# Performance work log

Measured on AMD Instinct MI355X. Metric: run time of the kernel, lower is better.

## Reference

```python
import jax, jax.numpy as jnp
import numpy as np

B, S, H = 4, 16, 4096          # batch, new query tokens, hidden
NH, NKV, HD = 32, 8, 128       # query heads, kv heads, head_dim
PAST = 8192                    # cached kv length
ROPE_BASE = 10000.0


def setup_inputs() -> dict:
    key = jax.random.key(0)
    ks = jax.random.split(key, 7)
    wscale = 0.02
    hidden_states = jax.random.normal(ks[0], (B, S, H), jnp.float32)
    k_cache = jax.random.normal(ks[1], (B, PAST, NKV, HD), jnp.float32)
    v_cache = jax.random.normal(ks[2], (B, PAST, NKV, HD), jnp.float32)
    Wq = jax.random.normal(ks[3], (H, NH * HD), jnp.float32) * wscale
    Wk = jax.random.normal(ks[4], (H, NKV * HD), jnp.float32) * wscale
    Wv = jax.random.normal(ks[5], (H, NKV * HD), jnp.float32) * wscale
    Wo = jax.random.normal(ks[6], (NH * HD, H), jnp.float32) * wscale
    position_ids = PAST + jnp.tile(jnp.arange(S, dtype=jnp.int32)[None, :], (B, 1))
    return {"hidden_states": hidden_states, "k_cache": k_cache, "v_cache": v_cache,
            "Wq": Wq, "Wk": Wk, "Wv": Wv, "Wo": Wo, "position_ids": position_ids}


def _rotate_half(x):
    h = x.shape[-1] // 2
    return jnp.concatenate([-x[..., h:], x[..., :h]], axis=-1)


def reference(hidden_states, k_cache, v_cache, Wq, Wk, Wv, Wo, position_ids):
    b, s, _ = hidden_states.shape
    # projections -> [b, heads, s, hd]
    q = (hidden_states @ Wq).reshape(b, s, NH, HD).transpose(0, 2, 1, 3)
    k = (hidden_states @ Wk).reshape(b, s, NKV, HD).transpose(0, 2, 1, 3)
    v = (hidden_states @ Wv).reshape(b, s, NKV, HD).transpose(0, 2, 1, 3)
    # RoPE (LlamaRotaryEmbedding: base=10000, half-split rotate)
    inv_freq = 1.0 / (ROPE_BASE ** (jnp.arange(0, HD, 2, dtype=jnp.float32) / HD))
    ang = position_ids.astype(jnp.float32)[..., None] * inv_freq      # [b, s, hd/2]
    emb = jnp.concatenate([ang, ang], axis=-1)                        # [b, s, hd]
    cos = jnp.cos(emb)[:, None]                                       # [b, 1, s, hd]
    sin = jnp.sin(emb)[:, None]
    q = q * cos + _rotate_half(q) * sin
    k = k * cos + _rotate_half(k) * sin
    # kv-cache concat: cache stored [b, past, nkv, hd] -> [b, nkv, K, hd]
    k_all = jnp.concatenate([k_cache.transpose(0, 2, 1, 3), k], axis=2)
    v_all = jnp.concatenate([v_cache.transpose(0, 2, 1, 3), v], axis=2)
    # GQA repeat_kv (repeat_interleave along head dim)
    n_rep = NH // NKV
    k_all = jnp.repeat(k_all, n_rep, axis=1)                          # [b, NH, K, hd]
    v_all = jnp.repeat(v_all, n_rep, axis=1)
    K = k_all.shape[2]
    scale = HD ** -0.5
    scores = jnp.einsum('bhqd,bhkd->bhqk', q, k_all) * scale          # [b, NH, s, K]
    # flash varlen causal with seqlen_q < seqlen_k: bottom-right aligned mask
    allow = jnp.arange(K)[None, :] <= (K - s + jnp.arange(s))[:, None]
    scores = jnp.where(allow, scores, jnp.float32(-1e30))
    probs = jax.nn.softmax(scores, axis=-1)
    attn = jnp.einsum('bhqk,bhkd->bhqd', probs, v_all)                # [b, NH, s, hd]
    attn = attn.transpose(0, 2, 1, 3).reshape(b, s, NH * HD)
    return attn @ Wo
```

## Files before the change

kernel.cpp:

```cpp
#include <hip/hip_runtime.h>

#define BB 4
#define SS 16
#define NH 32
#define NKV 8
#define HD 128
#define PAST 8192
#define KVLEN 8208
#define KSPLIT 8
#define ASPLIT 16
#define CHUNK 513
#define NTILE 9

typedef __attribute__((ext_vector_type(8))) short short8;
typedef __attribute__((ext_vector_type(4))) float f32x4;

__device__ __forceinline__ unsigned short f2bf(float f) {
  unsigned u = __float_as_uint(f);
  u = (u + 0x7FFFu + ((u >> 16) & 1u)) >> 16;
  return (unsigned short)u;
}
__device__ __forceinline__ float bf2f(unsigned short h) {
  return __uint_as_float(((unsigned)h) << 16);
}
__device__ __forceinline__ unsigned cvtpk(float lo, float hi) {
  unsigned r;
  asm("v_cvt_pk_bf16_f32 %0, %1, %2" : "=v"(r) : "v"(lo), "v"(hi));
  return r;
}
__device__ __forceinline__ void st8(void* p, unsigned lo, unsigned hi) {
  *(unsigned long long*)p = (unsigned long long)lo | ((unsigned long long)hi << 32);
}
__device__ __forceinline__ float getc(const float4& v, int c) {
  return c == 0 ? v.x : c == 1 ? v.y : c == 2 ? v.z : v.w;
}
__device__ __forceinline__ int imin(int a, int b) { return a < b ? a : b; }
__device__ __forceinline__ int imax(int a, int b) { return a > b ? a : b; }

__device__ __forceinline__ void bar_lds() {
  asm volatile("s_waitcnt lgkmcnt(0)" ::: "memory");
  __builtin_amdgcn_s_barrier();
  asm volatile("" ::: "memory");
}
__device__ __forceinline__ void wait_lds() {
  asm volatile("s_waitcnt lgkmcnt(0)" ::: "memory");
}

__global__ __launch_bounds__(256) void xconv(const float* __restrict__ X,
                                             unsigned short* __restrict__ XB) {
  int gid = blockIdx.x * 256 + threadIdx.x;
  float4 v = *(const float4*)&X[(size_t)gid * 4];
  ushort4 pk;
  pk.x = f2bf(v.x); pk.y = f2bf(v.y); pk.z = f2bf(v.z); pk.w = f2bf(v.w);
  *(ushort4*)&XB[(size_t)gid * 4] = pk;
}

__global__ __launch_bounds__(256) void gemm_skinny(
    const unsigned short* __restrict__ A,
    const float* __restrict__ W0, const float* __restrict__ W1, const float* __restrict__ W2,
    int nw0, int nw1, int nw2,
    float* __restrict__ part, int Ntot, int kchunk) {
  __shared__ unsigned short Wt[64 * 64];
  const int nt = blockIdx.x, ks = blockIdx.y;
  const int tid = threadIdx.x, lane = tid & 63, w = tid >> 6;
  const int lr = lane & 15, lc = lane >> 4;
  const int n0 = nt * 64;
  const float* W; int wld, wcol;
  if (n0 < nw0) { W = W0; wld = nw0; wcol = n0; }
  else if (n0 < nw0 + nw1) { W = W1; wld = nw1; wcol = n0 - nw0; }
  else { W = W2; wld = nw2; wcol = n0 - nw0 - nw1; }

  f32x4 acc[4];
  #pragma unroll
  for (int mi = 0; mi < 4; ++mi)
    #pragma unroll
    for (int i = 0; i < 4; ++i) acc[mi][i] = 0.f;

  const int qn = tid & 15, qk = tid >> 4;
  const int kb0 = ks * kchunk;
  const int nkt = kchunk / 64;

  float4 wr0, wr1, wr2, wr3;
  {
    const float* wp = &W[(size_t)(kb0 + qk * 4) * wld + wcol + qn * 4];
    wr0 = *(const float4*)(wp);
    wr1 = *(const float4*)(wp + wld);
    wr2 = *(const float4*)(wp + 2 * (size_t)wld);
    wr3 = *(const float4*)(wp + 3 * (size_t)wld);
  }

  for (int kt = 0; kt < nkt; ++kt) {
    const int kb = kb0 + kt * 64;
    #pragma unroll
    for (int c = 0; c < 4; ++c) {
      const int n = qn * 4 + c;
      ushort4 pk;
      pk.x = f2bf(getc(wr0, c)); pk.y = f2bf(getc(wr1, c));
      pk.z = f2bf(getc(wr2, c)); pk.w = f2bf(getc(wr3, c));
      const int byt = n * 128 + ((qk * 8) ^ ((n & 7) << 4));
      *(ushort4*)((char*)Wt + byt) = pk;
    }
    bar_lds();
    if (kt + 1 < nkt) {
      const float* wp = &W[(size_t)(kb + 64 + qk * 4) * wld + wcol + qn * 4];
      wr0 = *(const float4*)(wp);
      wr1 = *(const float4*)(wp + wld);
      wr2 = *(const float4*)(wp + 2 * (size_t)wld);
      wr3 = *(const float4*)(wp + 3 * (size_t)wld);
    }
    #pragma unroll
    for (int kh = 0; kh < 2; ++kh) {
      const int ncol = w * 16 + lr;
      short8 bf = *(const short8*)((char*)Wt + ncol * 128 + ((kh * 64 + lc * 16) ^ ((ncol & 7) << 4)));
      const int kkg = kb + kh * 32 + lc * 8;
      #pragma unroll
      for (int mi = 0; mi < 4; ++mi) {
        short8 af = *(const short8*)&A[(size_t)(mi * 16 + lr) * 4096 + kkg];
        acc[mi] = __builtin_amdgcn_mfma_f32_16x16x32_bf16(af, bf, acc[mi], 0, 0, 0);
      }
    }
    bar_lds();
  }
  #pragma unroll
  for (int mi = 0; mi < 4; ++mi)
    #pragma unroll
    for (int i = 0; i < 4; ++i) {
      const int row = mi * 16 + lc * 4 + i;
      part[((size_t)ks * 64 + row) * Ntot + n0 + w * 16 + lr] = acc[mi][i];
    }
}

__global__ __launch_bounds__(256) void proj_reduce(
    const float* __restrict__ part, const int* __restrict__ posids,
    unsigned short* __restrict__ QR, float* __restrict__ KF,
    float* __restrict__ VF) {
  __shared__ double sInv[64];
  const int tid = threadIdx.x;
  if (tid < 64)
    sInv[tid] = exp2(-(double)tid * (13.287712379549449 / 64.0));
  __syncthreads();

  const int gid = blockIdx.x * 256 + tid;
  const int j = gid & 63;
  const int hh = (gid >> 6) % 48;
  const int row = gid / 3072;
  const int b = row >> 4, s = row & 15;
  int col0; bool rope;
  if (hh < 32)      { col0 = hh * 128 + j; rope = true; }
  else if (hh < 40) { col0 = 4096 + (hh - 32) * 128 + j; rope = true; }
  else              { col0 = 5120 + (hh - 40) * 128 + j; rope = false; }
  float v0 = 0.f, v1 = 0.f;
  #pragma unroll
  for (int ks = 0; ks < KSPLIT; ++ks) {
    v0 += part[((size_t)ks * 64 + row) * 6144 + col0];
    v1 += part[((size_t)ks * 64 + row) * 6144 + col0 + 64];
  }
  float o0 = v0, o1 = v1;
  if (rope) {
    const int pos = posids[row];
    const double inv = sInv[j];
    double th = (double)pos * inv;
    const double TWO_PI = 6.283185307179586476925286766559;
    th -= floor(th / TWO_PI) * TWO_PI;
    float sv, cv;
    sincosf((float)th, &sv, &cv);
    o0 = v0 * cv - v1 * sv;
    o1 = v1 * cv + v0 * sv;
  }
  if (hh < 32) {
    const size_t didx = (((size_t)(b * 32 + hh) * 16 + s) * 128) + j;
    QR[didx] = f2bf(o0);
    QR[didx + 64] = f2bf(o1);
  } else if (hh < 40) {
    const size_t didx = (((size_t)(b * 8 + (hh - 32)) * 16 + s) * 128) + j;
    KF[didx] = o0;
    KF[didx + 64] = o1;
  } else {
    const size_t didx = (((size_t)(b * 8 + (hh - 40)) * 16 + s) * 128) + j;
    VF[didx] = o0;
    VF[didx + 64] = o1;
  }
}

__global__ __launch_bounds__(512, 2) void attn_kernel(
    const float* __restrict__ kc, const float* __restrict__ vc,
    const unsigned short* __restrict__ QR, const float* __restrict__ KF,
    const float* __restrict__ VF,
    float* __restrict__ Opart, float* __restrict__ ML) {
  __shared__ unsigned short Klds[2][64 * 136];
  __shared__ unsigned short Vt[2][128 * 64];
  __shared__ unsigned short Plds[4][16 * 72];

  const int kvh = blockIdx.x & 7, b = blockIdx.x >> 3;
  const int split = blockIdx.y;
  const int tid = threadIdx.x;
  const int kstart = split * CHUNK;

  if (tid >= 256) {
    const int ptid = tid - 256;
    const int dl = (ptid & 31) * 4;
    const int rk = ptid >> 5;
    const float* kc_base = kc + (((size_t)b * PAST) * NKV + kvh) * HD + dl;
    const float* vc_base = vc + (((size_t)b * PAST) * NKV + kvh) * HD + dl;
    const float* kf_base = KF + (((size_t)b * NKV + kvh) * SS) * HD + dl;
    const float* vf_base = VF + (((size_t)b * NKV + kvh) * SS) * HD + dl;

    auto stage = [&](int kk0, int buf) {
      float4 kpre[8];
      float4 vpre[8];
      #pragma unroll
      for (int pass = 0; pass < 8; ++pass) {
        const int kk = kk0 + pass * 8 + rk;
        const int ts = imin(imax(kk - PAST, 0), SS - 1);
        const float* p = (kk < PAST) ? (kc_base + (size_t)kk * (NKV * HD))
                                     : (kf_base + (size_t)ts * HD);
        kpre[pass] = *(const float4*)p;
      }
      #pragma unroll
      for (int j = 0; j < 8; ++j) {
        const int kk = kk0 + rk * 8 + j;
        const int ts = imin(imax(kk - PAST, 0), SS - 1);
        const float* p = (kk < PAST) ? (vc_base + (size_t)kk * (NKV * HD))
                                     : (vf_base + (size_t)ts * HD);
        vpre[j] = *(const float4*)p;
      }
      #pragma unroll
      for (int pass = 0; pass < 8; ++pass) {
        const int kr = pass * 8 + rk;
        st8((char*)&Klds[buf][0] + kr * 272 + dl * 2,
            cvtpk(kpre[pass].x, kpre[pass].y), cvtpk(kpre[pass].z, kpre[pass].w));
      }
      #pragma unroll
      for (int pp = 0; pp < 2; ++pp) {
        const int krb = rk * 8 + pp * 4;
        #pragma unroll
        for (int c = 0; c < 4; ++c) {
          const int d = dl + c;
          const int g = ((d ^ (d >> 3)) & 7) << 4;
          st8((char*)&Vt[buf][0] + d * 128 + ((krb * 2) ^ g),
              cvtpk(getc(vpre[pp * 4 + 0], c), getc(vpre[pp * 4 + 1], c)),
              cvtpk(getc(vpre[pp * 4 + 2], c), getc(vpre[pp * 4 + 3], c)));
        }
      }
    };

    stage(kstart, 0);
    bar_lds();
    for (int t = 0; t < NTILE; ++t) {
      if (t + 1 < NTILE) stage(kstart + (t + 1) * 64, (t + 1) & 1);
      bar_lds();
    }
  } else {
    const int lane = tid & 63, w = tid >> 6;
    const int lr = lane & 15, lc = lane >> 4;

    short8 qf[4];
    {
      const unsigned short* qb = QR + (((size_t)b * NH + kvh * 4 + w) * SS + lr) * HD;
      #pragma unroll
      for (int kd = 0; kd < 4; ++kd) qf[kd] = *(const short8*)(qb + kd * 32 + lc * 8);
    }

    float m_i[4], l_i[4];
    f32x4 oacc[8];
    #pragma unroll
    for (int i = 0; i < 4; ++i) { m_i[i] = -1e30f; l_i[i] = 0.f; }
    #pragma unroll
    for (int d8 = 0; d8 < 8; ++d8)
      #pragma unroll
      for (int i = 0; i < 4; ++i) oacc[d8][i] = 0.f;

    bar_lds();

    for (int t = 0; t < NTILE; ++t) {
      const int buf = t & 1;
      const int kk0 = kstart + t * 64;
      const int nvalid = imin(64, kstart + CHUNK - kk0);

      f32x4 sacc[4];
      #pragma unroll
      for (int nb = 0; nb < 4; ++nb)
        #pragma unroll
        for (int i = 0; i < 4; ++i) sacc[nb][i] = 0.f;
      #pragma unroll
      for (int kd = 0; kd < 4; ++kd) {
        #pragma unroll
        for (int nb = 0; nb < 4; ++nb) {
          const int key = nb * 16 + lr;
          short8 bf = *(const short8*)((char*)&Klds[buf][0] + key * 272 + kd * 64 + lc * 16);
          sacc[nb] = __builtin_amdgcn_mfma_f32_16x16x32_bf16(qf[kd], bf, sacc[nb], 0, 0, 0);
        }
      }

      const float scl = 0.08838834764831845f;
      float resc[4];
      #pragma unroll
      for (int i = 0; i < 4; ++i) {
        const int s = lc * 4 + i;
        float vv[4];
        #pragma unroll
        for (int nb = 0; nb < 4; ++nb) {
          const int klocal = nb * 16 + lr;
          const int kk = kk0 + klocal;
          const bool ok = (klocal < nvalid) && (kk <= PAST + s);
          vv[nb] = ok ? sacc[nb][i] * scl : -1e30f;
        }
        float mx = fmaxf(fmaxf(vv[0], vv[1]), fmaxf(vv[2], vv[3]));
        mx = fmaxf(mx, __shfl_xor(mx, 1));
        mx = fmaxf(mx, __shfl_xor(mx, 2));
        mx = fmaxf(mx, __shfl_xor(mx, 4));
        mx = fmaxf(mx, __shfl_xor(mx, 8));
        const float mnew = fmaxf(m_i[i], mx);
        const float rs = __expf(m_i[i] - mnew);
        float p0 = __expf(vv[0] - mnew), p1 = __expf(vv[1] - mnew);
        float p2 = __expf(vv[2] - mnew), p3 = __expf(vv[3] - mnew);
        float sum = p0 + p1 + p2 + p3;
        sum += __shfl_xor(sum, 1);
        sum += __shfl_xor(sum, 2);
        sum += __shfl_xor(sum, 4);
        sum += __shfl_xor(sum, 8);
        l_i[i] = l_i[i] * rs + sum;
        m_i[i] = mnew;
        resc[i] = rs;
        unsigned short* prow = &Plds[w][s * 72];
        prow[0 * 16 + lr] = f2bf(p0);
        prow[1 * 16 + lr] = f2bf(p1);
        prow[2 * 16 + lr] = f2bf(p2);
        prow[3 * 16 + lr] = f2bf(p3);
      }
      #pragma unroll
      for (int d8 = 0; d8 < 8; ++d8)
        #pragma unroll
        for (int i = 0; i < 4; ++i) oacc[d8][i] *= resc[i];

      wait_lds();

      #pragma unroll
      for (int ks2 = 0; ks2 < 2; ++ks2) {
        short8 pf = *(const short8*)((char*)&Plds[w][0] + lr * 144 + ks2 * 64 + lc * 16);
        #pragma unroll
        for (int db = 0; db < 8; ++db) {
          const int d = db * 16 + lr;
          const int g = ((d ^ (d >> 3)) & 7) << 4;
          short8 vf = *(const short8*)((char*)&Vt[buf][0] + d * 128 + ((ks2 * 64 + lc * 16) ^ g));
          oacc[db] = __builtin_amdgcn_mfma_f32_16x16x32_bf16(pf, vf, oacc[db], 0, 0, 0);
        }
      }

      bar_lds();
    }

    const size_t pbase = (((size_t)b * NKV + kvh) * ASPLIT + split) * 64;
    #pragma unroll
    for (int db = 0; db < 8; ++db)
      #pragma unroll
      for (int i = 0; i < 4; ++i) {
        const int row = w * 16 + lc * 4 + i;
        Opart[(pbase + row) * HD + db * 16 + lr] = oacc[db][i];
      }
    if (lr == 0) {
      #pragma unroll
      for (int i = 0; i < 4; ++i) {
        const int row = w * 16 + lc * 4 + i;
        ML[(pbase + row) * 2] = m_i[i];
        ML[(pbase + row) * 2 + 1] = l_i[i];
      }
    }
  }
}

__global__ __launch_bounds__(128) void combine(const float* __restrict__ Opart,
                                               const float* __restrict__ ML,
                                               unsigned short* __restrict__ AT) {
  const int rid = blockIdx.x;
  const int d = threadIdx.x;
  const int s = rid & 15, h = (rid >> 4) & 31, b = rid >> 9;
  const int kvh = h >> 2, g = h & 3;
  const int prow = g * 16 + s;
  const size_t base = ((size_t)b * NKV + kvh) * ASPLIT;
  float ms[ASPLIT], ls[ASPLIT];
  float M = -1e30f;
  #pragma unroll
  for (int sp = 0; sp < ASPLIT; ++sp) {
    ms[sp] = ML[((base + sp) * 64 + prow) * 2];
    ls[sp] = ML[((base + sp) * 64 + prow) * 2 + 1];
    M = fmaxf(M, ms[sp]);
  }
  float denom = 0.f, acc = 0.f;
  #pragma unroll
  for (int sp = 0; sp < ASPLIT; ++sp) {
    const float e = __expf(ms[sp] - M);
    denom += ls[sp] * e;
    acc += e * Opart[((base + sp) * 64 + prow) * HD + d];
  }
  AT[((size_t)(b * 16 + s)) * 4096 + h * 128 + d] = f2bf(acc / denom);
}

__global__ __launch_bounds__(256) void wo_reduce(const float* __restrict__ part,
                                                 float* __restrict__ out) {
  const int gid = blockIdx.x * 256 + threadIdx.x;
  float4 s = {0, 0, 0, 0};
  #pragma unroll
  for (int ks = 0; ks < KSPLIT; ++ks) {
    const float4 v = *(const float4*)&part[(size_t)ks * 262144 + (size_t)gid * 4];
    s.x += v.x; s.y += v.y; s.z += v.z; s.w += v.w;
  }
  *(float4*)&out[(size_t)gid * 4] = s;
}

extern "C" void kernel_launch(void* const* d_in, const int* in_sizes, int n_in,
                              void* d_out, int out_size, void* d_ws, size_t ws_size,
                              hipStream_t stream) {
  (void)in_sizes; (void)n_in; (void)out_size; (void)ws_size;
  const float* hs = (const float*)d_in[0];
  const float* kc = (const float*)d_in[1];
  const float* vc = (const float*)d_in[2];
  const float* Wq = (const float*)d_in[3];
  const float* Wk = (const float*)d_in[4];
  const float* Wv = (const float*)d_in[5];
  const float* Wo = (const float*)d_in[6];
  const int* pos = (const int*)d_in[7];
  float* out = (float*)d_out;
  char* ws = (char*)d_ws;

  unsigned short* XB = (unsigned short*)(ws);
  unsigned short* QR = (unsigned short*)(ws + 0x080000);
  float* KF = (float*)(ws + 0x100000);
  float* VF = (float*)(ws + 0x140000);
  unsigned short* AT = (unsigned short*)(ws + 0x180000);
  float* RED = (float*)(ws + 0x200000);
  float* ML  = (float*)(ws + 0x1300000);

  hipLaunchKernelGGL(xconv, dim3(256), dim3(256), 0, stream, hs, XB);
  hipLaunchKernelGGL(gemm_skinny, dim3(96, KSPLIT), dim3(256), 0, stream,
                     XB, Wq, Wk, Wv, 4096, 1024, 1024, RED, 6144, 4096 / KSPLIT);
  hipLaunchKernelGGL(proj_reduce, dim3(768), dim3(256), 0, stream, RED, pos, QR, KF, VF);
  hipLaunchKernelGGL(attn_kernel, dim3(NKV * BB, ASPLIT), dim3(512), 0, stream,
                     kc, vc, QR, KF, VF, RED, ML);
  hipLaunchKernelGGL(combine, dim3(2048), dim3(128), 0, stream, RED, ML, AT);
  hipLaunchKernelGGL(gemm_skinny, dim3(64, KSPLIT), dim3(256), 0, stream,
                     AT, Wo, Wo, Wo, 4096, 0, 0, RED, 4096, 4096 / KSPLIT);
  hipLaunchKernelGGL(wo_reduce, dim3(256), dim3(256), 0, stream, RED, out);
}
```

Baseline: 134.6 us.

## Restructure split-KV attention: 4 KV heads per block, 16-key tiles, 64 splits

The attention kernel is reorganised so each block handles four KV heads over a shorter key chunk (129 keys, 16-key tiles). The grid goes from 32x16 to 8x64 blocks, and each compute wave now owns one KV head and all four of its query heads. Partial outputs are stored as fp16 instead of fp32, which halves the partial-output traffic, and the combine kernel reduces over 64 splits instead of 16. The PV MFMA now has half of its K dimension zero-padded, which wastes tensor throughput. The extra splits also raise combine work and the ML read volume.

```diff
diff --git a/kernel.cpp b/kernel.cpp
--- a/kernel.cpp
+++ b/kernel.cpp
@@ -1,4 +1,5 @@
 #include <hip/hip_runtime.h>
+#include <hip/hip_fp16.h>
 
 #define BB 4
 #define SS 16
@@ -8,9 +9,9 @@
 #define PAST 8192
 #define KVLEN 8208
 #define KSPLIT 8
-#define ASPLIT 16
-#define CHUNK 513
-#define NTILE 9
+#define NSPLIT 64
+#define CHUNKK 129
+#define NT2 9
 
 typedef __attribute__((ext_vector_type(8))) short short8;
 typedef __attribute__((ext_vector_type(4))) float f32x4;
@@ -19,9 +20,6 @@
   unsigned u = __float_as_uint(f);
   u = (u + 0x7FFFu + ((u >> 16) & 1u)) >> 16;
   return (unsigned short)u;
-}
-__device__ __forceinline__ float bf2f(unsigned short h) {
-  return __uint_as_float(((unsigned)h) << 16);
 }
 __device__ __forceinline__ unsigned cvtpk(float lo, float hi) {
   unsigned r;
@@ -186,212 +184,228 @@
     const float* __restrict__ kc, const float* __restrict__ vc,
     const unsigned short* __restrict__ QR, const float* __restrict__ KF,
     const float* __restrict__ VF,
-    float* __restrict__ Opart, float* __restrict__ ML) {
-  __shared__ unsigned short Klds[2][64 * 136];
-  __shared__ unsigned short Vt[2][128 * 64];
-  __shared__ unsigned short Plds[4][16 * 72];
-
-  const int kvh = blockIdx.x & 7, b = blockIdx.x >> 3;
+    unsigned short* __restrict__ OP, float* __restrict__ ML) {
+  __shared__ unsigned short Klds[2][8192];
+  __shared__ unsigned short Vt[2][9248];
+  __shared__ unsigned short Plds[4][1280];
+
+  const int kvhq = blockIdx.x & 1, b = blockIdx.x >> 1;
   const int split = blockIdx.y;
   const int tid = threadIdx.x;
-  const int kstart = split * CHUNK;
+  const int kstart = split * CHUNKK;
+  const int kend = imin(kstart + CHUNKK, KVLEN);
+  const int vmax = kend - 1;
 
   if (tid >= 256) {
     const int ptid = tid - 256;
-    const int dl = (ptid & 31) * 4;
-    const int rk = ptid >> 5;
-    const float* kc_base = kc + (((size_t)b * PAST) * NKV + kvh) * HD + dl;
-    const float* vc_base = vc + (((size_t)b * PAST) * NKV + kvh) * HD + dl;
-    const float* kf_base = KF + (((size_t)b * NKV + kvh) * SS) * HD + dl;
-    const float* vf_base = VF + (((size_t)b * NKV + kvh) * SS) * HD + dl;
+    const int pw = ptid >> 6;
+    const int pl = ptid & 63;
+    const int lv = pl & 31;
+    const int hh2 = pl >> 5;
+    const int dd = lv * 4;
+
+    auto kaddr = [&](int kk, int kvl) -> const float* {
+      const int kkc = imin(kk, vmax);
+      const int kvh = kvhq * 4 + kvl;
+      if (kkc < PAST) return kc + (((size_t)b * PAST + kkc) * NKV + kvh) * HD + dd;
+      return KF + (((size_t)(b * NKV + kvh)) * SS + (kkc - PAST)) * HD + dd;
+    };
+    auto vaddr = [&](int kk, int kvl) -> const float* {
+      const int kkc = imin(kk, vmax);
+      const int kvh = kvhq * 4 + kvl;
+      if (kkc < PAST) return vc + (((size_t)b * PAST + kkc) * NKV + kvh) * HD + dd;
+      return VF + (((size_t)(b * NKV + kvh)) * SS + (kkc - PAST)) * HD + dd;
+    };
 
     auto stage = [&](int kk0, int buf) {
-      float4 kpre[8];
-      float4 vpre[8];
-      #pragma unroll
-      for (int pass = 0; pass < 8; ++pass) {
-        const int kk = kk0 + pass * 8 + rk;
-        const int ts = imin(imax(kk - PAST, 0), SS - 1);
-        const float* p = (kk < PAST) ? (kc_base + (size_t)kk * (NKV * HD))
-                                     : (kf_base + (size_t)ts * HD);
-        kpre[pass] = *(const float4*)p;
-      }
-      #pragma unroll
-      for (int j = 0; j < 8; ++j) {
-        const int kk = kk0 + rk * 8 + j;
-        const int ts = imin(imax(kk - PAST, 0), SS - 1);
-        const float* p = (kk < PAST) ? (vc_base + (size_t)kk * (NKV * HD))
-                                     : (vf_base + (size_t)ts * HD);
-        vpre[j] = *(const float4*)p;
-      }
-      #pragma unroll
-      for (int pass = 0; pass < 8; ++pass) {
-        const int kr = pass * 8 + rk;
-        st8((char*)&Klds[buf][0] + kr * 272 + dl * 2,
-            cvtpk(kpre[pass].x, kpre[pass].y), cvtpk(kpre[pass].z, kpre[pass].w));
-      }
-      #pragma unroll
-      for (int pp = 0; pp < 2; ++pp) {
-        const int krb = rk * 8 + pp * 4;
+      char* Kb = (char*)&Klds[buf][0];
+      char* Vb = (char*)&Vt[buf][0];
+      #pragma unroll
+      for (int j = 0; j < 4; ++j) {
+        const int key = pw * 4 + j;
+        #pragma unroll
+        for (int h = 0; h < 2; ++h) {
+          const int kvl = h * 2 + hh2;
+          float4 f = *(const float4*)kaddr(kk0 + key, kvl);
+          st8(Kb + (kvl * 16 + key) * 256 + ((dd * 2) ^ ((key & 7) << 4)),
+              cvtpk(f.x, f.y), cvtpk(f.z, f.w));
+        }
+      }
+      #pragma unroll
+      for (int h = 0; h < 2; ++h) {
+        const int kvl = h * 2 + hh2;
+        float4 r0 = *(const float4*)vaddr(kk0 + pw * 4 + 0, kvl);
+        float4 r1 = *(const float4*)vaddr(kk0 + pw * 4 + 1, kvl);
+        float4 r2 = *(const float4*)vaddr(kk0 + pw * 4 + 2, kvl);
+        float4 r3 = *(const float4*)vaddr(kk0 + pw * 4 + 3, kvl);
         #pragma unroll
         for (int c = 0; c < 4; ++c) {
-          const int d = dl + c;
-          const int g = ((d ^ (d >> 3)) & 7) << 4;
-          st8((char*)&Vt[buf][0] + d * 128 + ((krb * 2) ^ g),
-              cvtpk(getc(vpre[pp * 4 + 0], c), getc(vpre[pp * 4 + 1], c)),
-              cvtpk(getc(vpre[pp * 4 + 2], c), getc(vpre[pp * 4 + 3], c)));
+          const int byt = kvl * 4624 + c * 1156 + lv * 36 + pw * 8;
+          *(unsigned*)(Vb + byt)     = cvtpk(getc(r0, c), getc(r1, c));
+          *(unsigned*)(Vb + byt + 4) = cvtpk(getc(r2, c), getc(r3, c));
         }
       }
     };
 
     stage(kstart, 0);
     bar_lds();
-    for (int t = 0; t < NTILE; ++t) {
-      if (t + 1 < NTILE) stage(kstart + (t + 1) * 64, (t + 1) & 1);
+    for (int t = 0; t < NT2; ++t) {
+      if (t + 1 < NT2) stage(kstart + (t + 1) * 16, (t + 1) & 1);
       bar_lds();
     }
   } else {
     const int lane = tid & 63, w = tid >> 6;
     const int lr = lane & 15, lc = lane >> 4;
 
-    short8 qf[4];
-    {
-      const unsigned short* qb = QR + (((size_t)b * NH + kvh * 4 + w) * SS + lr) * HD;
-      #pragma unroll
-      for (int kd = 0; kd < 4; ++kd) qf[kd] = *(const short8*)(qb + kd * 32 + lc * 8);
-    }
-
-    float m_i[4], l_i[4];
-    f32x4 oacc[8];
-    #pragma unroll
-    for (int i = 0; i < 4; ++i) { m_i[i] = -1e30f; l_i[i] = 0.f; }
-    #pragma unroll
-    for (int d8 = 0; d8 < 8; ++d8)
-      #pragma unroll
-      for (int i = 0; i < 4; ++i) oacc[d8][i] = 0.f;
+    short8 qf[4][4];
+    #pragma unroll
+    for (int g = 0; g < 4; ++g) {
+      const unsigned short* qb =
+          QR + (((size_t)(b * 32 + (kvhq * 4 + w) * 4 + g)) * 16 + lr) * 128;
+      #pragma unroll
+      for (int kd = 0; kd < 4; ++kd) qf[g][kd] = *(const short8*)(qb + kd * 32 + lc * 8);
+    }
+
+    float m_i[4][4], l_i[4][4];
+    f32x4 oacc[4][8];
+    #pragma unroll
+    for (int g = 0; g < 4; ++g)
+      #pragma unroll
+      for (int i = 0; i < 4; ++i) { m_i[g][i] = -1e30f; l_i[g][i] = 0.f; }
+    #pragma unroll
+    for (int g = 0; g < 4; ++g)
+      #pragma unroll
+      for (int db = 0; db < 8; ++db)
+        #pragma unroll
+        for (int i = 0; i < 4; ++i) oacc[g][db][i] = 0.f;
 
     bar_lds();
 
-    for (int t = 0; t < NTILE; ++t) {
+    for (int t = 0; t < NT2; ++t) {
       const int buf = t & 1;
-      const int kk0 = kstart + t * 64;
-      const int nvalid = imin(64, kstart + CHUNK - kk0);
-
+      const int kk0 = kstart + t * 16;
+      const int nvalid = imin(16, kend - kk0);
+      const char* Kb = (const char*)&Klds[buf][0];
+      const char* Vb = (const char*)&Vt[buf][0] + w * 4624;
+
+      short8 bfk[4];
+      #pragma unroll
+      for (int kd = 0; kd < 4; ++kd)
+        bfk[kd] = *(const short8*)(Kb + (w * 16 + lr) * 256 +
+                                   ((kd * 64 + lc * 16) ^ ((lr & 7) << 4)));
       f32x4 sacc[4];
       #pragma unroll
-      for (int nb = 0; nb < 4; ++nb)
-        #pragma unroll
-        for (int i = 0; i < 4; ++i) sacc[nb][i] = 0.f;
-      #pragma unroll
-      for (int kd = 0; kd < 4; ++kd) {
-        #pragma unroll
-        for (int nb = 0; nb < 4; ++nb) {
-          const int key = nb * 16 + lr;
-          short8 bf = *(const short8*)((char*)&Klds[buf][0] + key * 272 + kd * 64 + lc * 16);
-          sacc[nb] = __builtin_amdgcn_mfma_f32_16x16x32_bf16(qf[kd], bf, sacc[nb], 0, 0, 0);
-        }
+      for (int g = 0; g < 4; ++g) {
+        #pragma unroll
+        for (int i = 0; i < 4; ++i) sacc[g][i] = 0.f;
+        #pragma unroll
+        for (int kd = 0; kd < 4; ++kd)
+          sacc[g] = __builtin_amdgcn_mfma_f32_16x16x32_bf16(qf[g][kd], bfk[kd], sacc[g], 0, 0, 0);
       }
 
       const float scl = 0.08838834764831845f;
-      float resc[4];
-      #pragma unroll
-      for (int i = 0; i < 4; ++i) {
-        const int s = lc * 4 + i;
-        float vv[4];
-        #pragma unroll
-        for (int nb = 0; nb < 4; ++nb) {
-          const int klocal = nb * 16 + lr;
-          const int kk = kk0 + klocal;
-          const bool ok = (klocal < nvalid) && (kk <= PAST + s);
-          vv[nb] = ok ? sacc[nb][i] * scl : -1e30f;
-        }
-        float mx = fmaxf(fmaxf(vv[0], vv[1]), fmaxf(vv[2], vv[3]));
-        mx = fmaxf(mx, __shfl_xor(mx, 1));
-        mx = fmaxf(mx, __shfl_xor(mx, 2));
-        mx = fmaxf(mx, __shfl_xor(mx, 4));
-        mx = fmaxf(mx, __shfl_xor(mx, 8));
-        const float mnew = fmaxf(m_i[i], mx);
-        const float rs = __expf(m_i[i] - mnew);
-        float p0 = __expf(vv[0] - mnew), p1 = __expf(vv[1] - mnew);
-        float p2 = __expf(vv[2] - mnew), p3 = __expf(vv[3] - mnew);
-        float sum = p0 + p1 + p2 + p3;
-        sum += __shfl_xor(sum, 1);
-        sum += __shfl_xor(sum, 2);
-        sum += __shfl_xor(sum, 4);
-        sum += __shfl_xor(sum, 8);
-        l_i[i] = l_i[i] * rs + sum;
-        m_i[i] = mnew;
-        resc[i] = rs;
-        unsigned short* prow = &Plds[w][s * 72];
-        prow[0 * 16 + lr] = f2bf(p0);
-        prow[1 * 16 + lr] = f2bf(p1);
-        prow[2 * 16 + lr] = f2bf(p2);
-        prow[3 * 16 + lr] = f2bf(p3);
-      }
-      #pragma unroll
-      for (int d8 = 0; d8 < 8; ++d8)
-        #pragma unroll
-        for (int i = 0; i < 4; ++i) oacc[d8][i] *= resc[i];
+      float resc[4][4];
+      #pragma unroll
+      for (int g = 0; g < 4; ++g)
+        #pragma unroll
+        for (int i = 0; i < 4; ++i) {
+          const int s = lc * 4 + i;
+          const bool ok = (lr < nvalid) && (kk0 + lr <= PAST + s);
+          const float vv = ok ? sacc[g][i] * scl : -1e30f;
+          float mx = vv;
+          mx = fmaxf(mx, __shfl_xor(mx, 1));
+          mx = fmaxf(mx, __shfl_xor(mx, 2));
+          mx = fmaxf(mx, __shfl_xor(mx, 4));
+          mx = fmaxf(mx, __shfl_xor(mx, 8));
+          const float mnew = fmaxf(m_i[g][i], mx);
+          const float rs = __expf(m_i[g][i] - mnew);
+          const float p = ok ? __expf(vv - mnew) : 0.f;
+          float sum = p;
+          sum += __shfl_xor(sum, 1);
+          sum += __shfl_xor(sum, 2);
+          sum += __shfl_xor(sum, 4);
+          sum += __shfl_xor(sum, 8);
+          l_i[g][i] = l_i[g][i] * rs + sum;
+          m_i[g][i] = mnew;
+          resc[g][i] = rs;
+          Plds[w][(g * 16 + s) * 20 + lr] = f2bf(p);
+        }
+      #pragma unroll
+      for (int g = 0; g < 4; ++g)
+        #pragma unroll
+        for (int db = 0; db < 8; ++db)
+          #pragma unroll
+          for (int i = 0; i < 4; ++i) oacc[g][db][i] *= resc[g][i];
 
       wait_lds();
 
-      #pragma unroll
-      for (int ks2 = 0; ks2 < 2; ++ks2) {
-        short8 pf = *(const short8*)((char*)&Plds[w][0] + lr * 144 + ks2 * 64 + lc * 16);
-        #pragma unroll
-        for (int db = 0; db < 8; ++db) {
-          const int d = db * 16 + lr;
-          const int g = ((d ^ (d >> 3)) & 7) << 4;
-          short8 vf = *(const short8*)((char*)&Vt[buf][0] + d * 128 + ((ks2 * 64 + lc * 16) ^ g));
-          oacc[db] = __builtin_amdgcn_mfma_f32_16x16x32_bf16(pf, vf, oacc[db], 0, 0, 0);
-        }
-      }
-
+      unsigned pfa[4], pfb[4];
+      #pragma unroll
+      for (int g = 0; g < 4; ++g) {
+        const char* pp = (const char*)&Plds[w][0] + (g * 16 + lr) * 40 + lc * 8;
+        pfa[g] = *(const unsigned*)pp;
+        pfb[g] = *(const unsigned*)(pp + 4);
+      }
+      #pragma unroll
+      for (int db = 0; db < 8; ++db) {
+        const int byt = (lr & 3) * 1156 + (db * 4 + (lr >> 2)) * 36 + lc * 8;
+        union { unsigned u[4]; short8 v; } vfu;
+        vfu.u[0] = *(const unsigned*)(Vb + byt);
+        vfu.u[1] = *(const unsigned*)(Vb + byt + 4);
+        vfu.u[2] = 0; vfu.u[3] = 0;
+        #pragma unroll
+        for (int g = 0; g < 4; ++g) {
+          union { unsigned u[4]; short8 v; } pfu;
+          pfu.u[0] = pfa[g]; pfu.u[1] = pfb[g]; pfu.u[2] = 0; pfu.u[3] = 0;
+          oacc[g][db] = __builtin_amdgcn_mfma_f32_16x16x32_bf16(pfu.v, vfu.v, oacc[g][db], 0, 0, 0);
+        }
+      }
       bar_lds();
     }
 
-    const size_t pbase = (((size_t)b * NKV + kvh) * ASPLIT + split) * 64;
-    #pragma unroll
-    for (int db = 0; db < 8; ++db)
-      #pragma unroll
-      for (int i = 0; i < 4; ++i) {
-        const int row = w * 16 + lc * 4 + i;
-        Opart[(pbase + row) * HD + db * 16 + lr] = oacc[db][i];
-      }
+    const size_t obase = (((size_t)(b * 2 + kvhq)) * NSPLIT + split) * 256;
+    #pragma unroll
+    for (int g = 0; g < 4; ++g)
+      #pragma unroll
+      for (int db = 0; db < 8; ++db)
+        #pragma unroll
+        for (int i = 0; i < 4; ++i) {
+          const int lrow = (w * 4 + g) * 16 + lc * 4 + i;
+          OP[(obase + lrow) * 128 + db * 16 + lr] =
+              __half_as_ushort(__float2half(oacc[g][db][i]));
+        }
     if (lr == 0) {
       #pragma unroll
-      for (int i = 0; i < 4; ++i) {
-        const int row = w * 16 + lc * 4 + i;
-        ML[(pbase + row) * 2] = m_i[i];
-        ML[(pbase + row) * 2 + 1] = l_i[i];
-      }
-    }
-  }
-}
-
-__global__ __launch_bounds__(128) void combine(const float* __restrict__ Opart,
+      for (int g = 0; g < 4; ++g)
+        #pragma unroll
+        for (int i = 0; i < 4; ++i) {
+          const int lrow = (w * 4 + g) * 16 + lc * 4 + i;
+          ML[(obase + lrow) * 2] = m_i[g][i];
+          ML[(obase + lrow) * 2 + 1] = l_i[g][i];
+        }
+    }
+  }
+}
+
+__global__ __launch_bounds__(128) void combine(const unsigned short* __restrict__ OP,
                                                const float* __restrict__ ML,
                                                unsigned short* __restrict__ AT) {
   const int rid = blockIdx.x;
   const int d = threadIdx.x;
   const int s = rid & 15, h = (rid >> 4) & 31, b = rid >> 9;
   const int kvh = h >> 2, g = h & 3;
-  const int prow = g * 16 + s;
-  const size_t base = ((size_t)b * NKV + kvh) * ASPLIT;
-  float ms[ASPLIT], ls[ASPLIT];
+  const int kvhq = kvh >> 2, kl = kvh & 3;
+  const int lrow = (kl * 4 + g) * 16 + s;
+  const size_t base = ((size_t)(b * 2 + kvhq)) * NSPLIT;
   float M = -1e30f;
-  #pragma unroll
-  for (int sp = 0; sp < ASPLIT; ++sp) {
-    ms[sp] = ML[((base + sp) * 64 + prow) * 2];
-    ls[sp] = ML[((base + sp) * 64 + prow) * 2 + 1];
-    M = fmaxf(M, ms[sp]);
-  }
+  for (int sp = 0; sp < NSPLIT; ++sp)
+    M = fmaxf(M, ML[((base + sp) * 256 + lrow) * 2]);
   float denom = 0.f, acc = 0.f;
-  #pragma unroll
-  for (int sp = 0; sp < ASPLIT; ++sp) {
-    const float e = __expf(ms[sp] - M);
-    denom += ls[sp] * e;
-    acc += e * Opart[((base + sp) * 64 + prow) * HD + d];
+  for (int sp = 0; sp < NSPLIT; ++sp) {
+    const size_t rbase = (base + sp) * 256 + lrow;
+    const float e = __expf(ML[rbase * 2] - M);
+    denom += ML[rbase * 2 + 1] * e;
+    acc += e * __half2float(__ushort_as_half(OP[rbase * 128 + d]));
   }
   AT[((size_t)(b * 16 + s)) * 4096 + h * 128 + d] = f2bf(acc / denom);
 }
@@ -429,15 +443,16 @@
   float* VF = (float*)(ws + 0x140000);
   unsigned short* AT = (unsigned short*)(ws + 0x180000);
   float* RED = (float*)(ws + 0x200000);
-  float* ML  = (float*)(ws + 0x1300000);
+  unsigned short* OP = (unsigned short*)(ws + 0x200000);
+  float* ML  = (float*)(ws + 0x2400000);
 
   hipLaunchKernelGGL(xconv, dim3(256), dim3(256), 0, stream, hs, XB);
   hipLaunchKernelGGL(gemm_skinny, dim3(96, KSPLIT), dim3(256), 0, stream,
                      XB, Wq, Wk, Wv, 4096, 1024, 1024, RED, 6144, 4096 / KSPLIT);
   hipLaunchKernelGGL(proj_reduce, dim3(768), dim3(256), 0, stream, RED, pos, QR, KF, VF);
-  hipLaunchKernelGGL(attn_kernel, dim3(NKV * BB, ASPLIT), dim3(512), 0, stream,
-                     kc, vc, QR, KF, VF, RED, ML);
-  hipLaunchKernelGGL(combine, dim3(2048), dim3(128), 0, stream, RED, ML, AT);
+  hipLaunchKernelGGL(attn_kernel, dim3(8, NSPLIT), dim3(512), 0, stream,
+                     kc, vc, QR, KF, VF, OP, ML);
+  hipLaunchKernelGGL(combine, dim3(2048), dim3(128), 0, stream, OP, ML, AT);
   hipLaunchKernelGGL(gemm_skinny, dim3(64, KSPLIT), dim3(256), 0, stream,
                      AT, Wo, Wo, Wo, 4096, 0, 0, RED, 4096, 4096 / KSPLIT);
   hipLaunchKernelGGL(wo_reduce, dim3(256), dim3(256), 0, stream, RED, out);
```

New measurement: 233.5 us. 73.4% more time.
